# Kernel optimization log

Measured on AMD Instinct MI355X. Metric: run time of the kernel, lower is better.

## Reference

```python
import jax, jax.numpy as jnp
import numpy as np

FEATURE_SIZE = 40960
FIRST_HIDDEN = 512
HALF = FIRST_HIDDEN // 2  # 256, per-perspective width
SECOND_HIDDEN = 32
BATCH = 4096


def setup_inputs() -> dict:
    key = jax.random.key(0)
    ks = jax.random.split(key, 10)
    inp = {
        "white_features": jax.random.uniform(ks[0], (BATCH, FEATURE_SIZE), dtype=jnp.float32),
        "black_features": jax.random.uniform(ks[1], (BATCH, FEATURE_SIZE), dtype=jnp.float32),
        # input_layer1 and input_layer2 share weight_float/bias_float -> single param
        "w_in": jax.random.normal(ks[2], (HALF, FEATURE_SIZE), dtype=jnp.float32) * 0.1,
        "b_in": jnp.zeros((HALF,), dtype=jnp.float32),
        "w_h1": jax.random.normal(ks[3], (SECOND_HIDDEN, FIRST_HIDDEN), dtype=jnp.float32) * 0.1,
        "b_h1": jnp.zeros((SECOND_HIDDEN,), dtype=jnp.float32),
        "w_h2": jax.random.normal(ks[4], (SECOND_HIDDEN, SECOND_HIDDEN), dtype=jnp.float32) * 0.1,
        "b_h2": jnp.zeros((SECOND_HIDDEN,), dtype=jnp.float32),
        "w_out": jax.random.normal(ks[5], (1, SECOND_HIDDEN), dtype=jnp.float32) * 0.1,
        "b_out": jnp.zeros((1,), dtype=jnp.float32),
    }
    return inp


def _clipped_relu(x):
    return jnp.clip(x, 0.0, 1.0)


def reference(white_features, black_features, w_in, b_in, w_h1, b_h1, w_h2, b_h2, w_out, b_out):
    # Perspective feature transform (shared weights), training-mode float path
    out1 = white_features @ w_in.T + b_in  # [B, 256]
    out2 = black_features @ w_in.T + b_in  # [B, 256]
    x = _clipped_relu(jnp.concatenate([out1, out2], axis=1))  # [B, 512]
    x = _clipped_relu(x @ w_h1.T + b_h1)  # [B, 32]
    x = _clipped_relu(x @ w_h2.T + b_h2)  # [B, 32]
    return x @ w_out.T + b_out  # [B, 1]
```

## Files before the change

kernel.cpp:

```cpp
#include <hip/hip_runtime.h>
#include <hip/hip_fp16.h>


#define FEAT 40960
#define PSTRIDE (8192ull * 256ull)
#define KSPLIT 8
#define KCHUNK (FEAT / KSPLIT)
#define NSTEPS (KCHUNK / 32)

using floatx4 = __attribute__((ext_vector_type(4))) float;
using half8   = __attribute__((ext_vector_type(8))) _Float16;
using half4   = __attribute__((ext_vector_type(4))) _Float16;

template <typename PT>
__global__ __launch_bounds__(512, 4) void nnue_gemm8(
    const float* __restrict__ white, const float* __restrict__ black,
    const float* __restrict__ w_in, PT* __restrict__ P)
{
    __shared__ __align__(16) _Float16 As[128 * 32];
    __shared__ __align__(16) _Float16 Ws[256 * 32];

    const int tid  = threadIdx.x;
    const int lane = tid & 63;
    const int wave = tid >> 6;
    const int wm   = wave >> 2;
    const int wn   = wave & 3;

    const int mb = blockIdx.x & 63;
    const int ks = blockIdx.x >> 6;

    const float* Abase = (mb < 32)
        ? (white + (size_t)mb * 128 * FEAT)
        : (black + (size_t)(mb - 32) * 128 * FEAT);
    const int k0 = ks * KCHUNK;

    const int c4    = tid & 7;
    const int row0  = tid >> 3;
    const int swz_w = (row0 & 3) << 4;

    const int frow  = lane & 15;
    const int fhi   = lane >> 4;
    const int swz_r = (frow & 3) << 4;

    floatx4 acc[4][4];
    const floatx4 zero = {0.f, 0.f, 0.f, 0.f};
#pragma unroll
    for (int m = 0; m < 4; ++m)
#pragma unroll
        for (int n = 0; n < 4; ++n) acc[m][n] = zero;

    floatx4 ra[2], rw[4];

    auto issue = [&](int kglob) {
#pragma unroll
        for (int i = 0; i < 2; ++i)
            ra[i] = *reinterpret_cast<const floatx4*>(
                Abase + (size_t)(row0 + 64 * i) * FEAT + kglob + c4 * 4);
#pragma unroll
        for (int i = 0; i < 4; ++i)
            rw[i] = *reinterpret_cast<const floatx4*>(
                w_in + (size_t)(row0 + 64 * i) * FEAT + kglob + c4 * 4);
    };

    auto cvtStore = [&]() {
        const int off = (c4 * 8) ^ swz_w;
#pragma unroll
        for (int i = 0; i < 2; ++i) {
            half4 h;
#pragma unroll
            for (int j = 0; j < 4; ++j) h[j] = (_Float16)ra[i][j];
            *reinterpret_cast<half4*>(
                reinterpret_cast<char*>(&As[0]) + (row0 + 64 * i) * 64 + off) = h;
        }
#pragma unroll
        for (int i = 0; i < 4; ++i) {
            half4 h;
#pragma unroll
            for (int j = 0; j < 4; ++j) h[j] = (_Float16)rw[i][j];
            *reinterpret_cast<half4*>(
                reinterpret_cast<char*>(&Ws[0]) + (row0 + 64 * i) * 64 + off) = h;
        }
    };

    auto mfmaStep = [&]() {
        const int kb = (fhi * 16) ^ swz_r;
        half8 bf[4];
#pragma unroll
        for (int n = 0; n < 4; ++n) {
            const int r = wn * 64 + n * 16 + frow;
            bf[n] = *reinterpret_cast<const half8*>(
                reinterpret_cast<const char*>(&Ws[0]) + r * 64 + kb);
        }
#pragma unroll
        for (int m = 0; m < 4; ++m) {
            const int r = wm * 64 + m * 16 + frow;
            half8 af = *reinterpret_cast<const half8*>(
                reinterpret_cast<const char*>(&As[0]) + r * 64 + kb);
#pragma unroll
            for (int n = 0; n < 4; ++n)
                acc[m][n] = __builtin_amdgcn_mfma_f32_16x16x32_f16(af, bf[n], acc[m][n], 0, 0, 0);
        }
    };

    issue(k0);
    for (int t = 0; t < NSTEPS; ++t) {
        cvtStore();
        if (t + 1 < NSTEPS) issue(k0 + (t + 1) * 32);
        __syncthreads();
        mfmaStep();
        __syncthreads();
    }

    PT* Pb = P + (size_t)ks * PSTRIDE + (size_t)mb * 128 * 256;
#pragma unroll
    for (int m = 0; m < 4; ++m)
#pragma unroll
        for (int n = 0; n < 4; ++n)
#pragma unroll
            for (int r = 0; r < 4; ++r) {
                const int row = wm * 64 + m * 16 + fhi * 4 + r;
                const int col = wn * 64 + n * 16 + frow;
                Pb[(size_t)row * 256 + col] = (PT)acc[m][n][r];
            }
}

template <typename PT>
__global__ __launch_bounds__(256) void nnue_tail8(
    const PT* __restrict__ P,
    const float* __restrict__ b_in,
    const float* __restrict__ w_h1, const float* __restrict__ b_h1,
    const float* __restrict__ w_h2, const float* __restrict__ b_h2,
    const float* __restrict__ w_out, const float* __restrict__ b_out,
    float* __restrict__ out)
{
    __shared__ float xs[32][512];
    __shared__ float w1[32][513];
    __shared__ float w2[32][33];
    __shared__ float h1[32][33];
    __shared__ float h2[32][33];
    __shared__ float wo[32];

    const int tid = threadIdx.x;
    const int b0  = blockIdx.x * 32;

    for (int i = tid; i < 32 * 512; i += 256) w1[i >> 9][i & 511] = w_h1[i];
    for (int i = tid; i < 32 * 32; i += 256)  w2[i >> 5][i & 31]  = w_h2[i];
    if (tid < 32) wo[tid] = w_out[tid];

    for (int i = tid; i < 32 * 512; i += 256) {
        const int r = i >> 9, c = i & 511;
        const int persp = c >> 8, n = c & 255;
        const size_t prow = (size_t)(b0 + r) + (persp ? 4096u : 0u);
        float v = 0.f;
#pragma unroll
        for (int s = 0; s < KSPLIT; ++s)
            v += (float)P[(size_t)s * PSTRIDE + prow * 256 + n];
        v += b_in[n];
        xs[r][c] = fminf(fmaxf(v, 0.f), 1.f);
    }
    __syncthreads();

    for (int p = tid; p < 32 * 32; p += 256) {
        const int o = p & 31, r = p >> 5;
        float a = b_h1[o];
        for (int j = 0; j < 512; ++j) a += xs[r][j] * w1[o][j];
        h1[r][o] = fminf(fmaxf(a, 0.f), 1.f);
    }
    __syncthreads();

    for (int p = tid; p < 32 * 32; p += 256) {
        const int o = p & 31, r = p >> 5;
        float a = b_h2[o];
        for (int j = 0; j < 32; ++j) a += h1[r][j] * w2[o][j];
        h2[r][o] = fminf(fmaxf(a, 0.f), 1.f);
    }
    __syncthreads();

    if (tid < 32) {
        float a = b_out[0];
        for (int j = 0; j < 32; ++j) a += h2[tid][j] * wo[j];
        out[b0 + tid] = a;
    }
}

__global__ __launch_bounds__(256) void nnue_naive(
    const float* __restrict__ white, const float* __restrict__ black,
    const float* __restrict__ w_in, const float* __restrict__ b_in,
    const float* __restrict__ w_h1, const float* __restrict__ b_h1,
    const float* __restrict__ w_h2, const float* __restrict__ b_h2,
    const float* __restrict__ w_out, const float* __restrict__ b_out,
    float* __restrict__ out)
{
    __shared__ float feat[4096];
    __shared__ float xs[512];
    __shared__ float h1s[32];
    __shared__ float h2s[32];
    const int b = blockIdx.x, tid = threadIdx.x;
    float acc0 = 0.f, acc1 = 0.f;
    for (int c = 0; c < FEAT; c += 2048) {
        for (int i = tid; i < 2048; i += 256) {
            feat[i]        = white[(size_t)b * FEAT + c + i];
            feat[2048 + i] = black[(size_t)b * FEAT + c + i];
        }
        __syncthreads();
        const float* wr = w_in + (size_t)tid * FEAT + c;
        for (int k = 0; k < 2048; ++k) {
            const float w = wr[k];
            acc0 += feat[k] * w;
            acc1 += feat[2048 + k] * w;
        }
        __syncthreads();
    }
    xs[tid]       = fminf(fmaxf(acc0 + b_in[tid], 0.f), 1.f);
    xs[256 + tid] = fminf(fmaxf(acc1 + b_in[tid], 0.f), 1.f);
    __syncthreads();
    if (tid < 32) {
        float a = b_h1[tid];
        for (int j = 0; j < 512; ++j) a += xs[j] * w_h1[tid * 512 + j];
        h1s[tid] = fminf(fmaxf(a, 0.f), 1.f);
    }
    __syncthreads();
    if (tid < 32) {
        float a = b_h2[tid];
        for (int j = 0; j < 32; ++j) a += h1s[j] * w_h2[tid * 32 + j];
        h2s[tid] = fminf(fmaxf(a, 0.f), 1.f);
    }
    __syncthreads();
    if (tid == 0) {
        float a = b_out[0];
        for (int j = 0; j < 32; ++j) a += h2s[j] * w_out[j];
        out[b] = a;
    }
}

extern "C" void kernel_launch(void* const* d_in, const int* in_sizes, int n_in,
                              void* d_out, int out_size, void* d_ws, size_t ws_size,
                              hipStream_t stream)
{
    const float* white = (const float*)d_in[0];
    const float* black = (const float*)d_in[1];
    const float* w_in  = (const float*)d_in[2];
    const float* b_in  = (const float*)d_in[3];
    const float* w_h1  = (const float*)d_in[4];
    const float* b_h1  = (const float*)d_in[5];
    const float* w_h2  = (const float*)d_in[6];
    const float* b_h2  = (const float*)d_in[7];
    const float* w_out = (const float*)d_in[8];
    const float* b_out = (const float*)d_in[9];
    float* out = (float*)d_out;

    const size_t f32Need = KSPLIT * PSTRIDE * sizeof(float);
    const size_t f16Need = KSPLIT * PSTRIDE * sizeof(_Float16);

    if (ws_size >= f32Need) {
        float* P = (float*)d_ws;
        nnue_gemm8<float><<<dim3(64 * KSPLIT), 512, 0, stream>>>(white, black, w_in, P);
        nnue_tail8<float><<<dim3(128), 256, 0, stream>>>(P, b_in, w_h1, b_h1,
                                                         w_h2, b_h2, w_out, b_out, out);
    } else if (ws_size >= f16Need) {
        _Float16* P = (_Float16*)d_ws;
        nnue_gemm8<_Float16><<<dim3(64 * KSPLIT), 512, 0, stream>>>(white, black, w_in, P);
        nnue_tail8<_Float16><<<dim3(128), 256, 0, stream>>>(P, b_in, w_h1, b_h1,
                                                            w_h2, b_h2, w_out, b_out, out);
    } else {
        nnue_naive<<<4096, 256, 0, stream>>>(white, black, w_in, b_in, w_h1, b_h1,
                                             w_h2, b_h2, w_out, b_out, out);
    }
}
```

Measured before the change: 418.0 us.

## Double-buffer LDS tiles and change swizzle to cut barriers per k-step

```diff
diff --git a/kernel.cpp b/kernel.cpp
--- a/kernel.cpp
+++ b/kernel.cpp
@@ -17,8 +17,8 @@
     const float* __restrict__ white, const float* __restrict__ black,
     const float* __restrict__ w_in, PT* __restrict__ P)
 {
-    __shared__ __align__(16) _Float16 As[128 * 32];
-    __shared__ __align__(16) _Float16 Ws[256 * 32];
+    __shared__ __align__(16) _Float16 As[2][128 * 32];
+    __shared__ __align__(16) _Float16 Ws[2][256 * 32];
 
     const int tid  = threadIdx.x;
     const int lane = tid & 63;
@@ -36,11 +36,13 @@
 
     const int c4    = tid & 7;
     const int row0  = tid >> 3;
-    const int swz_w = (row0 & 3) << 4;
+    const int swz_w = ((row0 >> 1) & 3) << 4;
+    const int woff  = (c4 * 8) ^ swz_w;
 
     const int frow  = lane & 15;
     const int fhi   = lane >> 4;
-    const int swz_r = (frow & 3) << 4;
+    const int swz_r = ((frow >> 1) & 3) << 4;
+    const int kb    = (fhi * 16) ^ swz_r;
 
     floatx4 acc[4][4];
     const floatx4 zero = {0.f, 0.f, 0.f, 0.f};
@@ -62,15 +64,14 @@
                 w_in + (size_t)(row0 + 64 * i) * FEAT + kglob + c4 * 4);
     };
 
-    auto cvtStore = [&]() {
-        const int off = (c4 * 8) ^ swz_w;
+    auto cvtStore = [&](int buf) {
 #pragma unroll
         for (int i = 0; i < 2; ++i) {
             half4 h;
 #pragma unroll
             for (int j = 0; j < 4; ++j) h[j] = (_Float16)ra[i][j];
             *reinterpret_cast<half4*>(
-                reinterpret_cast<char*>(&As[0]) + (row0 + 64 * i) * 64 + off) = h;
+                reinterpret_cast<char*>(&As[buf][0]) + (row0 + 64 * i) * 64 + woff) = h;
         }
 #pragma unroll
         for (int i = 0; i < 4; ++i) {
@@ -78,24 +79,23 @@
 #pragma unroll
             for (int j = 0; j < 4; ++j) h[j] = (_Float16)rw[i][j];
             *reinterpret_cast<half4*>(
-                reinterpret_cast<char*>(&Ws[0]) + (row0 + 64 * i) * 64 + off) = h;
+                reinterpret_cast<char*>(&Ws[buf][0]) + (row0 + 64 * i) * 64 + woff) = h;
         }
     };
 
-    auto mfmaStep = [&]() {
-        const int kb = (fhi * 16) ^ swz_r;
+    auto mfmaStep = [&](int buf) {
         half8 bf[4];
 #pragma unroll
         for (int n = 0; n < 4; ++n) {
             const int r = wn * 64 + n * 16 + frow;
             bf[n] = *reinterpret_cast<const half8*>(
-                reinterpret_cast<const char*>(&Ws[0]) + r * 64 + kb);
+                reinterpret_cast<const char*>(&Ws[buf][0]) + r * 64 + kb);
         }
 #pragma unroll
         for (int m = 0; m < 4; ++m) {
             const int r = wm * 64 + m * 16 + frow;
             half8 af = *reinterpret_cast<const half8*>(
-                reinterpret_cast<const char*>(&As[0]) + r * 64 + kb);
+                reinterpret_cast<const char*>(&As[buf][0]) + r * 64 + kb);
 #pragma unroll
             for (int n = 0; n < 4; ++n)
                 acc[m][n] = __builtin_amdgcn_mfma_f32_16x16x32_f16(af, bf[n], acc[m][n], 0, 0, 0);
@@ -103,11 +103,16 @@
     };
 
     issue(k0);
+    cvtStore(0);
+    issue(k0 + 32);
+    __syncthreads();
+
     for (int t = 0; t < NSTEPS; ++t) {
-        cvtStore();
-        if (t + 1 < NSTEPS) issue(k0 + (t + 1) * 32);
-        __syncthreads();
-        mfmaStep();
+        mfmaStep(t & 1);
+        if (t + 1 < NSTEPS) {
+            cvtStore((t + 1) & 1);
+            if (t + 2 < NSTEPS) issue(k0 + (t + 2) * 32);
+        }
         __syncthreads();
     }
 
```

Result: faster. 397.2 us (-5.0%).

## Pre-convert weights to fp16 tiles and triple-buffer them via direct global-to-LDS loads

Applied to the files above, without the earlier changes.

```diff
diff --git a/kernel.cpp b/kernel.cpp
--- a/kernel.cpp
+++ b/kernel.cpp
@@ -6,126 +6,158 @@
 #define PSTRIDE (8192ull * 256ull)
 #define KSPLIT 8
 #define KCHUNK (FEAT / KSPLIT)
-#define NSTEPS (KCHUNK / 32)
+#define NSTEP 160
+#define WTILE_BYTES 16384
+#define WWS_BYTES (1280ull * WTILE_BYTES)
 
 using floatx4 = __attribute__((ext_vector_type(4))) float;
 using half8   = __attribute__((ext_vector_type(8))) _Float16;
-using half4   = __attribute__((ext_vector_type(4))) _Float16;
+
+__global__ __launch_bounds__(256) void nnue_wprep(
+    const float* __restrict__ w_in, _Float16* __restrict__ Wws)
+{
+    const int bid = blockIdx.x;
+    const int T   = (bid & 7) * NSTEP + (bid >> 3);
+    char* base = (char*)Wws + (size_t)T * WTILE_BYTES;
+    const int tid = threadIdx.x;
+    const int kg0 = T * 32;
+#pragma unroll
+    for (int i = 0; i < 4; ++i) {
+        const int G = tid + i * 256;
+        const int r = G >> 2, g = G & 3;
+        const float* src = w_in + (size_t)r * FEAT + kg0 + g * 8;
+        floatx4 v0 = *reinterpret_cast<const floatx4*>(src);
+        floatx4 v1 = *reinterpret_cast<const floatx4*>(src + 4);
+        half8 h;
+#pragma unroll
+        for (int j = 0; j < 4; ++j) { h[j] = (_Float16)v0[j]; h[4 + j] = (_Float16)v1[j]; }
+        *reinterpret_cast<half8*>(base + r * 64 + ((g ^ ((r >> 1) & 3)) << 4)) = h;
+    }
+}
 
 template <typename PT>
-__global__ __launch_bounds__(512, 4) void nnue_gemm8(
+__global__ __launch_bounds__(512, 4) void nnue_gemm_v9(
     const float* __restrict__ white, const float* __restrict__ black,
-    const float* __restrict__ w_in, PT* __restrict__ P)
-{
-    __shared__ __align__(16) _Float16 As[128 * 32];
-    __shared__ __align__(16) _Float16 Ws[256 * 32];
+    const _Float16* __restrict__ Wws, PT* __restrict__ P)
+{
+    __shared__ __align__(16) _Float16 Ws[3][256 * 32];
 
     const int tid  = threadIdx.x;
     const int lane = tid & 63;
     const int wave = tid >> 6;
-    const int wm   = wave >> 2;
-    const int wn   = wave & 3;
-
-    const int mb = blockIdx.x & 63;
-    const int ks = blockIdx.x >> 6;
+
+    const int ks = blockIdx.x & 7;
+    const int mb = blockIdx.x >> 3;
 
     const float* Abase = (mb < 32)
         ? (white + (size_t)mb * 128 * FEAT)
         : (black + (size_t)(mb - 32) * 128 * FEAT);
     const int k0 = ks * KCHUNK;
 
-    const int c4    = tid & 7;
-    const int row0  = tid >> 3;
-    const int swz_w = (row0 & 3) << 4;
-
-    const int frow  = lane & 15;
-    const int fhi   = lane >> 4;
-    const int swz_r = (frow & 3) << 4;
-
-    floatx4 acc[4][4];
+    const int frow = lane & 15;
+    const int fhi  = lane >> 4;
+
+    const float* Aptr = Abase + (size_t)(wave * 16 + frow) * FEAT + fhi * 8 + k0;
+
+    const int kb = (fhi * 16) ^ (((frow >> 1) & 3) << 4);
+
+    const char* wsrc0 = (const char*)Wws + (size_t)(ks * NSTEP) * WTILE_BYTES
+                        + wave * 2048 + lane * 16;
+
+    floatx4 acc[16];
     const floatx4 zero = {0.f, 0.f, 0.f, 0.f};
 #pragma unroll
-    for (int m = 0; m < 4; ++m)
-#pragma unroll
-        for (int n = 0; n < 4; ++n) acc[m][n] = zero;
-
-    floatx4 ra[2], rw[4];
-
-    auto issue = [&](int kglob) {
-#pragma unroll
-        for (int i = 0; i < 2; ++i)
-            ra[i] = *reinterpret_cast<const floatx4*>(
-                Abase + (size_t)(row0 + 64 * i) * FEAT + kglob + c4 * 4);
-#pragma unroll
-        for (int i = 0; i < 4; ++i)
-            rw[i] = *reinterpret_cast<const floatx4*>(
-                w_in + (size_t)(row0 + 64 * i) * FEAT + kglob + c4 * 4);
+    for (int n = 0; n < 16; ++n) acc[n] = zero;
+
+    floatx4 raA0, raA1, raB0, raB1;
+
+    auto issueW = [&](int t, int wb) {
+        const char* g = wsrc0 + (size_t)t * WTILE_BYTES;
+        char* l = (char*)&Ws[wb][0] + wave * 2048;
+        __builtin_amdgcn_global_load_lds(
+            (const __attribute__((address_space(1))) unsigned int*)g,
+            (__attribute__((address_space(3))) unsigned int*)l, 16, 0, 0);
+        __builtin_amdgcn_global_load_lds(
+            (const __attribute__((address_space(1))) unsigned int*)(g + 1024),
+            (__attribute__((address_space(3))) unsigned int*)(l + 1024), 16, 0, 0);
     };
 
-    auto cvtStore = [&]() {
-        const int off = (c4 * 8) ^ swz_w;
-#pragma unroll
-        for (int i = 0; i < 2; ++i) {
-            half4 h;
-#pragma unroll
-            for (int j = 0; j < 4; ++j) h[j] = (_Float16)ra[i][j];
-            *reinterpret_cast<half4*>(
-                reinterpret_cast<char*>(&As[0]) + (row0 + 64 * i) * 64 + off) = h;
-        }
-#pragma unroll
-        for (int i = 0; i < 4; ++i) {
-            half4 h;
-#pragma unroll
-            for (int j = 0; j < 4; ++j) h[j] = (_Float16)rw[i][j];
-            *reinterpret_cast<half4*>(
-                reinterpret_cast<char*>(&Ws[0]) + (row0 + 64 * i) * 64 + off) = h;
+    auto cvt = [&](const floatx4& a0, const floatx4& a1) {
+        half8 h;
+#pragma unroll
+        for (int j = 0; j < 4; ++j) { h[j] = (_Float16)a0[j]; h[4 + j] = (_Float16)a1[j]; }
+        return h;
+    };
+
+    auto mfmaStep = [&](int wb, half8 af) {
+        const char* wbase = (const char*)&Ws[wb][0];
+#pragma unroll
+        for (int n = 0; n < 16; ++n) {
+            half8 bf = *reinterpret_cast<const half8*>(
+                wbase + (n * 16 + frow) * 64 + kb);
+            acc[n] = __builtin_amdgcn_mfma_f32_16x16x32_f16(af, bf, acc[n], 0, 0, 0);
         }
     };
 
-    auto mfmaStep = [&]() {
-        const int kb = (fhi * 16) ^ swz_r;
-        half8 bf[4];
-#pragma unroll
-        for (int n = 0; n < 4; ++n) {
-            const int r = wn * 64 + n * 16 + frow;
-            bf[n] = *reinterpret_cast<const half8*>(
-                reinterpret_cast<const char*>(&Ws[0]) + r * 64 + kb);
+    auto stepf = [&](int t, int wbW, int wbR,
+                     floatx4& c0, floatx4& c1, floatx4& n0, floatx4& n1) {
+        issueW(t + 2, wbW);
+        __builtin_amdgcn_sched_barrier(0);
+        n0 = *reinterpret_cast<const floatx4*>(Aptr + (size_t)(t + 1) * 32);
+        n1 = *reinterpret_cast<const floatx4*>(Aptr + (size_t)(t + 1) * 32 + 4);
+        half8 af = cvt(c0, c1);
+        mfmaStep(wbR, af);
+        asm volatile("s_waitcnt vmcnt(4) lgkmcnt(0)" ::: "memory");
+        __builtin_amdgcn_s_barrier();
+        __builtin_amdgcn_sched_barrier(0);
+    };
+
+    issueW(0, 0);
+    issueW(1, 1);
+    __builtin_amdgcn_sched_barrier(0);
+    raA0 = *reinterpret_cast<const floatx4*>(Aptr);
+    raA1 = *reinterpret_cast<const floatx4*>(Aptr + 4);
+    asm volatile("s_waitcnt vmcnt(4)" ::: "memory");
+    __builtin_amdgcn_s_barrier();
+    __builtin_amdgcn_sched_barrier(0);
+
+    for (int tb = 0; tb < 156; tb += 6) {
+        stepf(tb + 0, 2, 0, raA0, raA1, raB0, raB1);
+        stepf(tb + 1, 0, 1, raB0, raB1, raA0, raA1);
+        stepf(tb + 2, 1, 2, raA0, raA1, raB0, raB1);
+        stepf(tb + 3, 2, 0, raB0, raB1, raA0, raA1);
+        stepf(tb + 4, 0, 1, raA0, raA1, raB0, raB1);
+        stepf(tb + 5, 1, 2, raB0, raB1, raA0, raA1);
+    }
+    stepf(156, 2, 0, raA0, raA1, raB0, raB1);
+    stepf(157, 0, 1, raB0, raB1, raA0, raA1);
+    raB0 = *reinterpret_cast<const floatx4*>(Aptr + (size_t)159 * 32);
+    raB1 = *reinterpret_cast<const floatx4*>(Aptr + (size_t)159 * 32 + 4);
+    {
+        half8 af = cvt(raA0, raA1);
+        mfmaStep(2, af);
+    }
+    asm volatile("s_waitcnt vmcnt(4) lgkmcnt(0)" ::: "memory");
+    __builtin_amdgcn_s_barrier();
+    __builtin_amdgcn_sched_barrier(0);
+    {
+        half8 af = cvt(raB0, raB1);
+        mfmaStep(0, af);
+    }
+
+    PT* Pb = P + (size_t)ks * PSTRIDE + (size_t)mb * 128 * 256;
+#pragma unroll
+    for (int n = 0; n < 16; ++n)
+#pragma unroll
+        for (int r = 0; r < 4; ++r) {
+            const int row = wave * 16 + fhi * 4 + r;
+            const int col = n * 16 + frow;
+            Pb[(size_t)row * 256 + col] = (PT)acc[n][r];
         }
-#pragma unroll
-        for (int m = 0; m < 4; ++m) {
-            const int r = wm * 64 + m * 16 + frow;
-            half8 af = *reinterpret_cast<const half8*>(
-                reinterpret_cast<const char*>(&As[0]) + r * 64 + kb);
-#pragma unroll
-            for (int n = 0; n < 4; ++n)
-                acc[m][n] = __builtin_amdgcn_mfma_f32_16x16x32_f16(af, bf[n], acc[m][n], 0, 0, 0);
-        }
-    };
-
-    issue(k0);
-    for (int t = 0; t < NSTEPS; ++t) {
-        cvtStore();
-        if (t + 1 < NSTEPS) issue(k0 + (t + 1) * 32);
-        __syncthreads();
-        mfmaStep();
-        __syncthreads();
-    }
-
-    PT* Pb = P + (size_t)ks * PSTRIDE + (size_t)mb * 128 * 256;
-#pragma unroll
-    for (int m = 0; m < 4; ++m)
-#pragma unroll
-        for (int n = 0; n < 4; ++n)
-#pragma unroll
-            for (int r = 0; r < 4; ++r) {
-                const int row = wm * 64 + m * 16 + fhi * 4 + r;
-                const int col = wn * 64 + n * 16 + frow;
-                Pb[(size_t)row * 256 + col] = (PT)acc[m][n][r];
-            }
 }
 
 template <typename PT>
-__global__ __launch_bounds__(256) void nnue_tail8(
+__global__ __launch_bounds__(256) void nnue_tail(
     const PT* __restrict__ P,
     const float* __restrict__ b_in,
     const float* __restrict__ w_h1, const float* __restrict__ b_h1,
@@ -249,19 +281,23 @@
     const float* b_out = (const float*)d_in[9];
     float* out = (float*)d_out;
 
-    const size_t f32Need = KSPLIT * PSTRIDE * sizeof(float);
-    const size_t f16Need = KSPLIT * PSTRIDE * sizeof(_Float16);
-
-    if (ws_size >= f32Need) {
+    const size_t pF32 = KSPLIT * PSTRIDE * sizeof(float);
+    const size_t pF16 = KSPLIT * PSTRIDE * sizeof(_Float16);
+
+    if (ws_size >= pF32 + WWS_BYTES) {
         float* P = (float*)d_ws;
-        nnue_gemm8<float><<<dim3(64 * KSPLIT), 512, 0, stream>>>(white, black, w_in, P);
-        nnue_tail8<float><<<dim3(128), 256, 0, stream>>>(P, b_in, w_h1, b_h1,
-                                                         w_h2, b_h2, w_out, b_out, out);
-    } else if (ws_size >= f16Need) {
+        _Float16* Wws = (_Float16*)((char*)d_ws + pF32);
+        nnue_wprep<<<dim3(1280), 256, 0, stream>>>(w_in, Wws);
+        nnue_gemm_v9<float><<<dim3(512), 512, 0, stream>>>(white, black, Wws, P);
+        nnue_tail<float><<<dim3(128), 256, 0, stream>>>(P, b_in, w_h1, b_h1,
+                                                        w_h2, b_h2, w_out, b_out, out);
+    } else if (ws_size >= pF16 + WWS_BYTES) {
         _Float16* P = (_Float16*)d_ws;
-        nnue_gemm8<_Float16><<<dim3(64 * KSPLIT), 512, 0, stream>>>(white, black, w_in, P);
-        nnue_tail8<_Float16><<<dim3(128), 256, 0, stream>>>(P, b_in, w_h1, b_h1,
-                                                            w_h2, b_h2, w_out, b_out, out);
+        _Float16* Wws = (_Float16*)((char*)d_ws + pF16);
+        nnue_wprep<<<dim3(1280), 256, 0, stream>>>(w_in, Wws);
+        nnue_gemm_v9<_Float16><<<dim3(512), 512, 0, stream>>>(white, black, Wws, P);
+        nnue_tail<_Float16><<<dim3(128), 256, 0, stream>>>(P, b_in, w_h1, b_h1,
+                                                           w_h2, b_h2, w_out, b_out, out);
     } else {
         nnue_naive<<<4096, 256, 0, stream>>>(white, black, w_in, b_in, w_h1, b_h1,
                                              w_h2, b_h2, w_out, b_out, out);
```

After: 393.9 us. -5.8%, faster.
